# Optimization experiments

Hardware: AMD Instinct MI355X
Metric: run time of the kernel (lower is better)

Reference implementation:

```python
import jax, jax.numpy as jnp
import numpy as np
from jax import lax

V, D, H, K, B, T = 32000, 300, 300, 9, 64, 512


def _lstm_dir(x, w_ih, w_hh, b_ih, b_hh, h0, c0):
    # x: [B, T, D]; torch gate order: i, f, g, o
    def step(carry, xt):
        h, c = carry
        gates = xt @ w_ih.T + h @ w_hh.T + b_ih + b_hh  # [B, 4H]
        i, f, g, o = jnp.split(gates, 4, axis=-1)
        i, f, o = jax.nn.sigmoid(i), jax.nn.sigmoid(f), jax.nn.sigmoid(o)
        g = jnp.tanh(g)
        c = f * c + i * g
        h = o * jnp.tanh(c)
        return (h, c), h

    xs = jnp.transpose(x, (1, 0, 2))  # [T, B, D]
    _, hs = lax.scan(step, (h0, c0), xs)
    return jnp.transpose(hs, (1, 0, 2))  # [B, T, H]


def _emissions(tokens, emb, w_ih_f, w_hh_f, b_ih_f, b_hh_f,
               w_ih_b, w_hh_b, b_ih_b, b_hh_b, h0, c0, w_out, b_out):
    x = emb[tokens]  # [B, T, D]
    hf = _lstm_dir(x, w_ih_f, w_hh_f, b_ih_f, b_hh_f, h0[0], c0[0])
    hb = _lstm_dir(jnp.flip(x, axis=1), w_ih_b, w_hh_b, b_ih_b, b_hh_b, h0[1], c0[1])
    hb = jnp.flip(hb, axis=1)
    out = jnp.concatenate([hf, hb], axis=-1)  # [B, T, 2H]
    return out @ w_out.T + b_out  # [B, T, K]


def _crf_nll(emissions, tags, mask, start_t, end_t, trans):
    # torchcrf: -sum_b log p(tags | emissions)
    e = jnp.transpose(emissions, (1, 0, 2))  # [T, B, K]
    tg = tags.T                               # [T, B]
    m = mask.T.astype(emissions.dtype)        # [T, B]
    bidx = jnp.arange(tags.shape[0])
    # numerator: gold path score
    num = start_t[tg[0]] + e[0][bidx, tg[0]]
    def nstep(carry, inp):
        et, tt, tp, mt = inp
        return carry + (trans[tp, tt] + et[bidx, tt]) * mt, None
    num, _ = lax.scan(nstep, num, (e[1:], tg[1:], tg[:-1], m[1:]))
    last_idx = mask.sum(axis=1).astype(jnp.int32) - 1
    last_tags = tags[bidx, last_idx]
    num = num + end_t[last_tags]
    # denominator: forward algorithm
    alpha = start_t + e[0]  # [B, K]
    def dstep(alpha, inp):
        et, mt = inp
        nxt = jax.scipy.special.logsumexp(alpha[:, :, None] + trans[None], axis=1) + et
        return jnp.where(mt[:, None] > 0, nxt, alpha), None
    alpha, _ = lax.scan(dstep, alpha, (e[1:], m[1:]))
    den = jax.scipy.special.logsumexp(alpha + end_t, axis=1)
    return -jnp.sum(num - den)


def _viterbi(emissions, mask, start_t, end_t, trans):
    e = jnp.transpose(emissions, (1, 0, 2))  # [T, B, K]
    m = mask.T                               # [T, B]
    score = start_t + e[0]                   # [B, K]
    def fstep(score, inp):
        et, mt = inp
        br = score[:, :, None] + trans[None]  # [B, K_prev, K_next]
        best = br.max(axis=1)
        idx = br.argmax(axis=1).astype(jnp.int32)  # [B, K]
        new = best + et
        return jnp.where(mt[:, None], new, score), idx
    score, history = lax.scan(fstep, score, (e[1:], m[1:]))  # history: [T-1, B, K]
    score = score + end_t
    last = jnp.argmax(score, axis=-1).astype(jnp.int32)  # [B]
    def bstep(tag, inp):
        idx_t, mt = inp
        prev = jnp.take_along_axis(idx_t, tag[:, None], axis=1)[:, 0]
        tag = jnp.where(mt, prev, tag)
        return tag, tag
    _, tags_rev = lax.scan(bstep, last, (history, m[1:]), reverse=True)  # [T-1, B]
    path = jnp.concatenate([tags_rev, last[None]], axis=0)  # [T, B]
    return path.T  # [B, T]


def setup_inputs() -> dict:
    key = jax.random.key(0)
    ks = jax.random.split(key, 20)
    s = 0.1
    emb = jax.random.normal(ks[0], (V, D), jnp.float32) * s
    emb = emb.at[0].set(0.0)  # padding_idx row
    inp = {
        "tokens": jax.random.randint(ks[1], (B, T), 0, V, jnp.int32),
        "tags": jax.random.randint(ks[2], (B, T), 0, K, jnp.int32),
        "mask": jnp.ones((B, T), jnp.bool_),
        "emb": emb,
        "w_ih_f": jax.random.normal(ks[3], (4 * H, D), jnp.float32) * s,
        "w_hh_f": jax.random.normal(ks[4], (4 * H, H), jnp.float32) * s,
        "b_ih_f": jax.random.normal(ks[5], (4 * H,), jnp.float32) * s,
        "b_hh_f": jax.random.normal(ks[6], (4 * H,), jnp.float32) * s,
        "w_ih_b": jax.random.normal(ks[7], (4 * H, D), jnp.float32) * s,
        "w_hh_b": jax.random.normal(ks[8], (4 * H, H), jnp.float32) * s,
        "b_ih_b": jax.random.normal(ks[9], (4 * H,), jnp.float32) * s,
        "b_hh_b": jax.random.normal(ks[10], (4 * H,), jnp.float32) * s,
        "h0": jax.random.normal(ks[11], (2, B, H), jnp.float32),
        "c0": jax.random.normal(ks[12], (2, B, H), jnp.float32),
        "w_out": jax.random.normal(ks[13], (K, 2 * H), jnp.float32) * s,
        "b_out": jax.random.normal(ks[14], (K,), jnp.float32) * s,
        "start_t": jax.random.normal(ks[15], (K,), jnp.float32) * s,
        "end_t": jax.random.normal(ks[16], (K,), jnp.float32) * s,
        "trans": jax.random.normal(ks[17], (K, K), jnp.float32) * s,
    }
    return inp


def reference(tokens, tags, mask, emb, w_ih_f, w_hh_f, b_ih_f, b_hh_f,
              w_ih_b, w_hh_b, b_ih_b, b_hh_b, h0, c0, w_out, b_out,
              start_t, end_t, trans):
    feats = _emissions(tokens, emb, w_ih_f, w_hh_f, b_ih_f, b_hh_f,
                       w_ih_b, w_hh_b, b_ih_b, b_hh_b, h0, c0, w_out, b_out)
    paths = _viterbi(feats, mask, start_t, end_t, trans)
    loss = _crf_nll(feats, tags, mask, start_t, end_t, trans)
    return paths, loss
```

## Files before the change

### kernel.cpp

```cpp
#include <hip/hip_runtime.h>
#include <math.h>

#define NV 32000
#define ND 300
#define NH 300
#define NK 9
#define NB 64
#define NT 512

typedef short bf16x8 __attribute__((ext_vector_type(8)));
typedef float f32x4  __attribute__((ext_vector_type(4)));

__device__ inline short bf16r(float x) {
    return (short)((__float_as_uint(x) + 0x8000u) >> 16);
}

__device__ inline float tanh_fast(float x) {
    float e2 = __expf(2.f * x);
    return 1.f - 2.f / (e2 + 1.f);
}

#define WB_OFF   0ull
#define WB_F     768000ull
#define E_OFF    (WB_OFF + WB_F)
#define E_SZ     ((unsigned long long)NT*NB*NK)
#define CBUF_OFF (E_OFF + E_SZ)
#define CBUF_SZ  (2ull*NB*NH)
#define HSLOT_OFF (CBUF_OFF + CBUF_SZ)
#define HSLOT_SZ  (2ull*2*NB*NH)
#define XP_OFF   (HSLOT_OFF + HSLOT_SZ)
#define XPC_SZ   (2ull*64*1200*64)
#define EB_OFF   (XP_OFF + XPC_SZ)
#define EB_SZ    (32000ull*320/2)
#define WS_NEED_EB ((EB_OFF + EB_SZ)*4ull)

__global__ __launch_bounds__(256) void k_wcvt(
    const float* __restrict__ wihf, const float* __restrict__ wihb,
    const float* __restrict__ whhf, const float* __restrict__ whhb,
    short* __restrict__ dst)
{
    int i = blockIdx.x*256 + threadIdx.x;
    if (i >= 1536000) return;
    int d  = i / 384000;
    int r2 = i % 384000;
    int j  = r2 / 320, k = r2 % 320;
    const float* src = (d == 0) ? wihf : (d == 1) ? wihb : (d == 2) ? whhf : whhb;
    float v = (k < 300) ? src[(size_t)j*300 + k] : 0.f;
    dst[i] = bf16r(v);
}

__global__ __launch_bounds__(256) void k_ecvt(
    const float* __restrict__ emb, short* __restrict__ dst)
{
    int i = blockIdx.x*256 + threadIdx.x;
    if (i >= 32000*320) return;
    int row = i / 320, col = i % 320;
    float v = (col < 300) ? emb[(size_t)row*300 + col] : 0.f;
    dst[i] = bf16r(v);
}

__global__ __launch_bounds__(256) void k_xproj(
    const int* __restrict__ tokens, const float* __restrict__ emb,
    const short* __restrict__ eb16, int use_eb,
    const short* __restrict__ wb16,
    const float* __restrict__ bif, const float* __restrict__ bhf,
    const float* __restrict__ bib, const float* __restrict__ bhb,
    float* __restrict__ xpc, int chunk)
{
    const int tid = threadIdx.x;
    const int w  = tid >> 6, L = tid & 63;
    const int lm = L & 15, lq = L >> 4;
    const int dir = blockIdx.z;
    const int m0 = blockIdx.x*128 + w*32;
    const int n0 = blockIdx.y*80;
    const int tbase = dir ? (448 - chunk*64) : (chunk*64);

    int tok[2];
#pragma unroll
    for (int mi = 0; mi < 2; ++mi) {
        int m = m0 + mi*16 + lm;
        int b = m >> 6, lt = m & 63;
        tok[mi] = tokens[b*512 + tbase + lt];
    }
    const short* brow[5];
#pragma unroll
    for (int ni = 0; ni < 5; ++ni) {
        int j = n0 + ni*16 + lm;
        brow[ni] = wb16 + ((size_t)dir*1200 + j)*320;
    }

    f32x4 acc[2][5];
#pragma unroll
    for (int mi = 0; mi < 2; ++mi)
#pragma unroll
        for (int ni = 0; ni < 5; ++ni)
#pragma unroll
            for (int r = 0; r < 4; ++r) acc[mi][ni][r] = 0.f;

    if (use_eb) {
        const short* arow[2];
#pragma unroll
        for (int mi = 0; mi < 2; ++mi) arow[mi] = eb16 + (size_t)tok[mi]*320;
        for (int k0 = 0; k0 < 320; k0 += 32) {
            const int kk = k0 + lq*8;
            bf16x8 af[2], bf[5];
#pragma unroll
            for (int mi = 0; mi < 2; ++mi)
                af[mi] = *(const bf16x8*)(arow[mi] + kk);
#pragma unroll
            for (int ni = 0; ni < 5; ++ni)
                bf[ni] = *(const bf16x8*)(brow[ni] + kk);
#pragma unroll
            for (int mi = 0; mi < 2; ++mi)
#pragma unroll
                for (int ni = 0; ni < 5; ++ni)
                    acc[mi][ni] = __builtin_amdgcn_mfma_f32_16x16x32_bf16(
                                      af[mi], bf[ni], acc[mi][ni], 0, 0, 0);
        }
    } else {
        const float* arow[2];
#pragma unroll
        for (int mi = 0; mi < 2; ++mi) arow[mi] = emb + (size_t)tok[mi]*300;
        const float4 z4 = make_float4(0.f,0.f,0.f,0.f);
        for (int k0 = 0; k0 < 320; k0 += 32) {
            const int kk = k0 + lq*8;
            bf16x8 af[2], bf[5];
#pragma unroll
            for (int mi = 0; mi < 2; ++mi) {
                float4 f1 = (kk   < 300) ? *(const float4*)(arow[mi] + kk)     : z4;
                float4 f2 = (kk+4 < 300) ? *(const float4*)(arow[mi] + kk + 4) : z4;
                af[mi][0]=bf16r(f1.x); af[mi][1]=bf16r(f1.y); af[mi][2]=bf16r(f1.z); af[mi][3]=bf16r(f1.w);
                af[mi][4]=bf16r(f2.x); af[mi][5]=bf16r(f2.y); af[mi][6]=bf16r(f2.z); af[mi][7]=bf16r(f2.w);
            }
#pragma unroll
            for (int ni = 0; ni < 5; ++ni)
                bf[ni] = *(const bf16x8*)(brow[ni] + kk);
#pragma unroll
            for (int mi = 0; mi < 2; ++mi)
#pragma unroll
                for (int ni = 0; ni < 5; ++ni)
                    acc[mi][ni] = __builtin_amdgcn_mfma_f32_16x16x32_bf16(
                                      af[mi], bf[ni], acc[mi][ni], 0, 0, 0);
        }
    }

#pragma unroll
    for (int ni = 0; ni < 5; ++ni) {
        int j = n0 + ni*16 + lm;
        int g = j/300, rr = j%300;
        int slc = rr/20, ul = rr%20;
        float bias = dir ? (bib[j]+bhb[j]) : (bif[j]+bhf[j]);
#pragma unroll
        for (int mi = 0; mi < 2; ++mi) {
#pragma unroll
            for (int r = 0; r < 4; ++r) {
                int m = m0 + mi*16 + lq*4 + r;
                int b = m >> 6, lt = m & 63;
                int sp = dir ? (63 - lt) : lt;
                size_t idx = ((((size_t)dir*64 + sp)*8 + (b>>3))*15 + slc)*640
                           + (size_t)(b&7)*80 + g*20 + ul;
                xpc[idx] = acc[mi][ni][r] + bias;
            }
        }
    }
}

__global__ __launch_bounds__(256) void k_rnn(
    const float* __restrict__ xpc,
    const short* __restrict__ whh16,
    const float* __restrict__ h0,
    unsigned* hslot, float* __restrict__ cbuf,
    float* __restrict__ ev, const float* __restrict__ wout,
    int s_begin, int s_count)
{
    __shared__ __align__(16) short h_sh16[16*328];
    __shared__ __align__(16) float xp_sh[640];
    __shared__ __align__(16) float gates_sh[80*9];
    __shared__ __align__(16) float wo_sh[180];
    __shared__ __align__(16) float hloc[160];

    const int tid = threadIdx.x;
    const int wv  = tid >> 6, L = tid & 63;
    const int lm  = L & 15, lq = L >> 4;
    const int dir = blockIdx.x / 120;
    const int rem = blockIdx.x % 120;
    const int sl  = rem / 8;
    const int gb  = rem % 8;
    const int u0  = sl * 20;

    const int tb = (wv == 0) ? 0 : (wv + 1);
    const int tn = (wv == 0) ? 2 : 1;

    bf16x8 A[2][10];
#pragma unroll 2
    for (int mt = 0; mt < 2; ++mt) {
        if (mt < tn) {
            int r = (tb + mt)*16 + lm;
            int grow = (r/20)*300 + u0 + (r%20);
            const short* wr = whh16 + ((size_t)dir*1200 + grow)*320;
#pragma unroll
            for (int ks = 0; ks < 10; ++ks)
                A[mt][ks] = *(const bf16x8*)(wr + ks*32 + lq*8);
        }
    }
    if (tid < 180) wo_sh[tid] = wout[(tid/20)*600 + dir*300 + u0 + (tid%20)];

    for (int i = tid; i < 16*328; i += 256) h_sh16[i] = 0;

    const bool isPW = (tid < 160);
    const int bl_p = tid/20, lu_p = tid%20;
    float c_reg = 0.f;
    if (isPW) c_reg = cbuf[((size_t)dir*NB + gb*8 + bl_p)*NH + u0 + lu_p];

    __syncthreads();

    for (int s = s_begin; s < s_begin + s_count; ++s) {
        const int t = dir ? (511 - s) : s;
        const int sp = s - s_begin;

        unsigned vb[10];
        unsigned* hsrc = hslot + (((size_t)(s & 1)*2 + dir)*NB + gb*8)*NH;
        if (s > 0 && tid < 240) {
#pragma unroll
            for (int j = 0; j < 10; ++j) {
                int i = tid + 256*j;
                if (i < 2400)
                    vb[j] = __hip_atomic_load(hsrc + i, __ATOMIC_RELAXED,
                                              __HIP_MEMORY_SCOPE_AGENT);
            }
        }

        {
            const float* xsrc = xpc + ((((size_t)dir*64 + sp)*8 + gb)*15 + sl)*640;
            if (tid < 160) *(float4*)(&xp_sh[tid*4]) = *(const float4*)(xsrc + tid*4);
        }

        if (s == 0) {
            const float* h0p = h0 + ((size_t)dir*NB + gb*8)*NH;
            for (int i = tid; i < 2400; i += 256)
                h_sh16[(i/300)*328 + (i%300)] = bf16r(h0p[i]);
        } else if (tid < 240) {
            const unsigned tg = (unsigned)s & 0xFFFFu;
            bool ok = false;
            while (!ok) {
                ok = true;
#pragma unroll
                for (int j = 0; j < 10; ++j) {
                    int i = tid + 256*j;
                    if (i < 2400 && (vb[j] >> 16) != tg) {
                        ok = false;
                        vb[j] = __hip_atomic_load(hsrc + i, __ATOMIC_RELAXED,
                                                  __HIP_MEMORY_SCOPE_AGENT);
                    }
                }
            }
#pragma unroll
            for (int j = 0; j < 10; ++j) {
                int i = tid + 256*j;
                if (i < 2400)
                    h_sh16[(i/300)*328 + (i%300)] = (short)(vb[j] & 0xFFFFu);
            }
        }
        __syncthreads();

        {
            bf16x8 Bf[10];
#pragma unroll
            for (int ks = 0; ks < 10; ++ks)
                Bf[ks] = *(const bf16x8*)(h_sh16 + lm*328 + ks*32 + lq*8);
            f32x4 acc[2];
#pragma unroll 2
            for (int mt = 0; mt < 2; ++mt) {
                if (mt < tn) {
#pragma unroll
                    for (int r = 0; r < 4; ++r) acc[mt][r] = 0.f;
#pragma unroll
                    for (int ks = 0; ks < 10; ++ks)
                        acc[mt] = __builtin_amdgcn_mfma_f32_16x16x32_bf16(
                                      A[mt][ks], Bf[ks], acc[mt], 0, 0, 0);
                    if (lm < 8) {
#pragma unroll
                        for (int r = 0; r < 4; ++r)
                            gates_sh[((tb+mt)*16 + lq*4 + r)*9 + lm] = acc[mt][r];
                    }
                }
            }
        }
        __syncthreads();

        if (isPW) {
            float G[4];
#pragma unroll
            for (int g = 0; g < 4; ++g)
                G[g] = xp_sh[bl_p*80 + g*20 + lu_p] + gates_sh[(g*20 + lu_p)*9 + bl_p];
            float ig = 1.f/(1.f+__expf(-G[0]));
            float fg = 1.f/(1.f+__expf(-G[1]));
            float gg = tanh_fast(G[2]);
            float og = 1.f/(1.f+__expf(-G[3]));
            c_reg = fg*c_reg + ig*gg;
            float h = og*tanh_fast(c_reg);
            unsigned hb = (__float_as_uint(h) + 0x8000u) >> 16;
            unsigned pk = (((unsigned)(s+1) & 0xFFFFu) << 16) | hb;
            __hip_atomic_store(
                &hslot[(((size_t)((s+1)&1)*2 + dir)*NB + gb*8 + bl_p)*NH + u0 + lu_p],
                pk, __ATOMIC_RELAXED, __HIP_MEMORY_SCOPE_AGENT);
            hloc[bl_p*20 + lu_p] = h;
        }
        __syncthreads();

        if (tid < 72) {
            int b = tid/9, k = tid%9;
            float a = 0.f;
#pragma unroll
            for (int u = 0; u < 20; ++u) a += hloc[b*20+u]*wo_sh[k*20+u];
            atomicAdd(&ev[((size_t)t*NB + gb*8 + b)*NK + k], a);
        }
    }

    if (isPW) cbuf[((size_t)dir*NB + gb*8 + bl_p)*NH + u0 + lu_p] = c_reg;
}

#define BT_C 14
#define BT_L 37

__global__ __launch_bounds__(128) void k_crf(
    const float* __restrict__ ev, const int* __restrict__ tags,
    const float* __restrict__ start_t, const float* __restrict__ end_t,
    const float* __restrict__ trans, const float* __restrict__ bout,
    float* __restrict__ out)
{
    __shared__ __align__(16) float ex_a[12];
    __shared__ __align__(16) float ex_v[12];
    __shared__ int hist_sh[511*NK];
    __shared__ int fmap[BT_C*NK];
    __shared__ int entry_sh[BT_C];
    __shared__ int last_sh;

    const int b = blockIdx.x, tid = threadIdx.x;
    const int wv = tid >> 6, ln = tid & 63;

    if (wv == 0) {
        float part = 0.f;
        for (int t = ln; t < NT; t += 64) {
            int tc = tags[b*NT + t];
            float e = ev[((size_t)t*NB + b)*NK + tc] + bout[tc];
            float pre = (t == 0) ? start_t[tc] : trans[tags[b*NT + t - 1]*9 + tc];
            part += pre + e;
        }
        if (ln == 63) part += end_t[tags[b*NT + NT - 1]];
#pragma unroll
        for (int off = 32; off > 0; off >>= 1)
            part += __shfl_down(part, off, 64);
        const float num = part;

        if (ln < 9) {
            const int kc = ln;
            float Tc[9];
#pragma unroll
            for (int kp = 0; kp < 9; ++kp) Tc[kp] = __expf(trans[kp*9 + kc]);
            const float bo = bout[kc];
            ex_a[kc] = start_t[kc] + ev[(size_t)b*NK + kc] + bo;
            float etn = ev[((size_t)1*NB + b)*NK + kc] + bo;

            for (int t = 1; t < NT; ++t) {
                float et = etn;
                if (t + 1 < NT) etn = ev[((size_t)(t+1)*NB + b)*NK + kc] + bo;

                float4 s0 = *(const float4*)(&ex_a[0]);
                float4 s1 = *(const float4*)(&ex_a[4]);
                float  a8 = ex_a[8];
                float a0=s0.x,a1=s0.y,a2=s0.z,a3=s0.w,a4=s1.x,a5=s1.y,a6=s1.z,a7=s1.w;

                float M = fmaxf(fmaxf(fmaxf(a0,a1),fmaxf(a2,a3)),
                                fmaxf(fmaxf(a4,a5),fmaxf(a6,a7)));
                M = fmaxf(M, a8);
                float s =        __expf(a0-M)*Tc[0];
                s = fmaf(__expf(a1-M), Tc[1], s);
                s = fmaf(__expf(a2-M), Tc[2], s);
                s = fmaf(__expf(a3-M), Tc[3], s);
                s = fmaf(__expf(a4-M), Tc[4], s);
                s = fmaf(__expf(a5-M), Tc[5], s);
                s = fmaf(__expf(a6-M), Tc[6], s);
                s = fmaf(__expf(a7-M), Tc[7], s);
                s = fmaf(__expf(a8-M), Tc[8], s);
                ex_a[kc] = M + __logf(s) + et;
            }

            if (ln == 0) {
                float M = -1e30f;
#pragma unroll
                for (int k = 0; k < 9; ++k) M = fmaxf(M, ex_a[k] + end_t[k]);
                float ls = 0.f;
#pragma unroll
                for (int k = 0; k < 9; ++k) ls += __expf(ex_a[k] + end_t[k] - M);
                float den = M + __logf(ls);
                atomicAdd(out + NB*NT, den - num);
            }
        }
    } else {
        if (ln < 9) {
            const int kc = ln;
            float Tc[9];
#pragma unroll
            for (int kp = 0; kp < 9; ++kp) Tc[kp] = trans[kp*9 + kc];
            const float bo = bout[kc];
            ex_v[kc] = start_t[kc] + ev[(size_t)b*NK + kc] + bo;
            float etn = ev[((size_t)1*NB + b)*NK + kc] + bo;

            for (int t = 1; t < NT; ++t) {
                float et = etn;
                if (t + 1 < NT) etn = ev[((size_t)(t+1)*NB + b)*NK + kc] + bo;

                float4 s0 = *(const float4*)(&ex_v[0]);
                float4 s1 = *(const float4*)(&ex_v[4]);
                float  a8 = ex_v[8];
                float a0=s0.x,a1=s0.y,a2=s0.z,a3=s0.w,a4=s1.x,a5=s1.y,a6=s1.z,a7=s1.w;

                float bv = a0 + Tc[0]; int arg = 0;
                float v;
                v = a1+Tc[1]; if (v > bv) { bv = v; arg = 1; }
                v = a2+Tc[2]; if (v > bv) { bv = v; arg = 2; }
                v = a3+Tc[3]; if (v > bv) { bv = v; arg = 3; }
                v = a4+Tc[4]; if (v > bv) { bv = v; arg = 4; }
                v = a5+Tc[5]; if (v > bv) { bv = v; arg = 5; }
                v = a6+Tc[6]; if (v > bv) { bv = v; arg = 6; }
                v = a7+Tc[7]; if (v > bv) { bv = v; arg = 7; }
                v = a8+Tc[8]; if (v > bv) { bv = v; arg = 8; }
                hist_sh[(t-1)*NK + kc] = arg;
                ex_v[kc] = bv + et;
            }

            if (ln == 0) {
                float best = -1e30f; int last = 0;
#pragma unroll
                for (int k = 0; k < 9; ++k) {
                    float v = ex_v[k] + end_t[k];
                    if (v > best) { best = v; last = k; }
                }
                last_sh = last;
            }
        }
    }

    __syncthreads();

    if (tid < BT_C*NK) {
        int c = tid / NK, s = tid % NK;
        int lo = c*BT_L, hi = min(511, lo + BT_L);
        int pos = s;
        for (int i = hi - 1; i >= lo; --i) pos = hist_sh[i*NK + pos];
        fmap[c*NK + s] = pos;
    }
    __syncthreads();
    if (tid == 0) {
        int e = last_sh;
        entry_sh[BT_C-1] = e;
        for (int c = BT_C - 2; c >= 0; --c) {
            e = fmap[(c+1)*NK + e];
            entry_sh[c] = e;
        }
    }
    __syncthreads();
    int* pout = (int*)out;
    if (tid < BT_C) {
        int c = tid;
        int lo = c*BT_L, hi = min(511, lo + BT_L);
        int pos = entry_sh[c];
        for (int i = hi - 1; i >= lo; --i) {
            pos = hist_sh[i*NK + pos];
            pout[b*NT + i] = pos;
        }
    }
    if (tid == 0) pout[b*NT + NT - 1] = last_sh;
}

extern "C" void kernel_launch(void* const* d_in, const int* in_sizes, int n_in,
                              void* d_out, int out_size, void* d_ws, size_t ws_size,
                              hipStream_t stream)
{
    (void)in_sizes; (void)n_in;

    const int*   tokens = (const int*)  d_in[0];
    const int*   tags   = (const int*)  d_in[1];
    const float* emb    = (const float*)d_in[3];
    const float* wihf   = (const float*)d_in[4];
    const float* whhf   = (const float*)d_in[5];
    const float* bihf   = (const float*)d_in[6];
    const float* bhhf   = (const float*)d_in[7];
    const float* wihb   = (const float*)d_in[8];
    const float* whhb   = (const float*)d_in[9];
    const float* bib    = (const float*)d_in[10];
    const float* bhhb   = (const float*)d_in[11];
    const float* h0     = (const float*)d_in[12];
    const float* c0     = (const float*)d_in[13];
    const float* wout   = (const float*)d_in[14];
    const float* bout   = (const float*)d_in[15];
    const float* startt = (const float*)d_in[16];
    const float* endt   = (const float*)d_in[17];
    const float* trans  = (const float*)d_in[18];

    float* ws    = (float*)d_ws;
    short* wb16  = (short*)(ws + WB_OFF);
    short* whh16 = wb16 + 768000;
    float* evp   = ws + E_OFF;
    float* cbuf  = ws + CBUF_OFF;
    unsigned* hslot = (unsigned*)(ws + HSLOT_OFF);
    float* xp    = ws + XP_OFF;
    short* eb16  = (short*)(ws + EB_OFF);
    float* out   = (float*)d_out;

    const int use_eb = (ws_size >= WS_NEED_EB) ? 1 : 0;

    (void)hipMemsetAsync(d_out, 0, (size_t)out_size * sizeof(float), stream);
    (void)hipMemsetAsync(evp, 0, (size_t)E_SZ * sizeof(float), stream);
    (void)hipMemcpyAsync(cbuf, c0, 2ull*NB*NH*sizeof(float), hipMemcpyDeviceToDevice, stream);

    k_wcvt<<<6000, 256, 0, stream>>>(wihf, wihb, whhf, whhb, wb16);
    if (use_eb)
        k_ecvt<<<40000, 256, 0, stream>>>(emb, eb16);

    for (int c = 0; c < 8; ++c) {
        k_xproj<<<dim3(32, 15, 2), 256, 0, stream>>>(
            tokens, emb, eb16, use_eb, wb16, bihf, bhhf, bib, bhhb, xp, c);
        k_rnn<<<240, 256, 0, stream>>>(
            xp, whh16, h0, hslot, cbuf, evp, wout, c*64, 64);
    }
    k_crf<<<64, 128, 0, stream>>>(evp, tags, startt, endt, trans, bout, out);
}
```

Before: 1.876 ms.

## Parallelize CRF forward and Viterbi recursions over time chunks with transfer matrices

Splits the 511-step CRF forward (logsumexp) and Viterbi (max-plus) recursions into 8 time chunks of 64 steps. Each chunk computes a 9x9 transfer matrix in parallel, one thread per start state. A single thread then composes the chunk matrices, and each chunk's Viterbi is replayed from the composed entry scores to fill the backpointer history in parallel. This targets the serial latency of the CRF kernel, but adds roughly 9x redundant arithmetic per chunk and an extra replay pass. It also doubles the block size to 256 threads.

```diff
diff --git a/kernel.cpp b/kernel.cpp
--- a/kernel.cpp
+++ b/kernel.cpp
@@ -322,98 +322,221 @@
 
 #define BT_C 14
 #define BT_L 37
-
-__global__ __launch_bounds__(128) void k_crf(
+#define CC 8
+#define CL 64
+
+__global__ __launch_bounds__(256) void k_crf(
     const float* __restrict__ ev, const int* __restrict__ tags,
     const float* __restrict__ start_t, const float* __restrict__ end_t,
     const float* __restrict__ trans, const float* __restrict__ bout,
     float* __restrict__ out)
 {
-    __shared__ __align__(16) float ex_a[12];
-    __shared__ __align__(16) float ex_v[12];
     __shared__ int hist_sh[511*NK];
+    __shared__ float Mlse[CC*81];
+    __shared__ float Mvit[CC*81];
+    __shared__ float entry_v[CC*9];
+    __shared__ __align__(16) float ex3[CC*12];
+    __shared__ float num_sh[256];
     __shared__ int fmap[BT_C*NK];
     __shared__ int entry_sh[BT_C];
     __shared__ int last_sh;
 
     const int b = blockIdx.x, tid = threadIdx.x;
-    const int wv = tid >> 6, ln = tid & 63;
-
-    if (wv == 0) {
+    const int wv = tid >> 6;
+
+    {
         float part = 0.f;
-        for (int t = ln; t < NT; t += 64) {
+        for (int t = tid; t < NT; t += 256) {
             int tc = tags[b*NT + t];
             float e = ev[((size_t)t*NB + b)*NK + tc] + bout[tc];
             float pre = (t == 0) ? start_t[tc] : trans[tags[b*NT + t - 1]*9 + tc];
             part += pre + e;
-        }
-        if (ln == 63) part += end_t[tags[b*NT + NT - 1]];
-#pragma unroll
-        for (int off = 32; off > 0; off >>= 1)
-            part += __shfl_down(part, off, 64);
-        const float num = part;
-
-        if (ln < 9) {
-            const int kc = ln;
+            if (t == NT - 1) part += end_t[tc];
+        }
+        num_sh[tid] = part;
+    }
+
+    {
+        int c = -1, j0 = 0, sr = 0;
+        if (wv == 0)      { if (tid < 63)        { c = tid/9;        j0 = tid%9;        sr = 0; } }
+        else if (wv == 1) { if (tid-64 < 63)     { c = (tid-64)/9;   j0 = (tid-64)%9;   sr = 1; } }
+        else if (wv == 2) { if (tid-128 < 9)     { c = 7;            j0 = tid-128;      sr = 0; } }
+        else              { if (tid-192 < 9)     { c = 7;            j0 = tid-192;      sr = 1; } }
+
+        if (c >= 0 && sr == 0) {
+            float Te[9][9];
+#pragma unroll
+            for (int i = 0; i < 9; ++i)
+#pragma unroll
+                for (int j = 0; j < 9; ++j) Te[i][j] = __expf(trans[i*9 + j]);
+            float bo[9];
+#pragma unroll
+            for (int j = 0; j < 9; ++j) bo[j] = bout[j];
+            float a[9];
+#pragma unroll
+            for (int j = 0; j < 9; ++j) a[j] = (j == j0) ? 0.f : -1e30f;
+            const int t0 = 1 + c*CL;
+            float etn[9];
+#pragma unroll
+            for (int j = 0; j < 9; ++j)
+                etn[j] = ev[((size_t)t0*NB + b)*NK + j] + bo[j];
+            for (int k = 0; k < CL; ++k) {
+                int t = t0 + k;
+                if (t >= NT) break;
+                float et[9];
+#pragma unroll
+                for (int j = 0; j < 9; ++j) et[j] = etn[j];
+                if (t + 1 < NT) {
+#pragma unroll
+                    for (int j = 0; j < 9; ++j)
+                        etn[j] = ev[((size_t)(t+1)*NB + b)*NK + j] + bo[j];
+                }
+                float M = a[0];
+#pragma unroll
+                for (int i = 1; i < 9; ++i) M = fmaxf(M, a[i]);
+                float p[9];
+#pragma unroll
+                for (int i = 0; i < 9; ++i) p[i] = __expf(a[i] - M);
+#pragma unroll
+                for (int j = 0; j < 9; ++j) {
+                    float s = p[0]*Te[0][j];
+#pragma unroll
+                    for (int i = 1; i < 9; ++i) s = fmaf(p[i], Te[i][j], s);
+                    a[j] = M + __logf(s) + et[j];
+                }
+            }
+#pragma unroll
+            for (int j = 0; j < 9; ++j) Mlse[c*81 + j0*9 + j] = a[j];
+        } else if (c >= 0) {
+            float Tv[9][9];
+#pragma unroll
+            for (int i = 0; i < 9; ++i)
+#pragma unroll
+                for (int j = 0; j < 9; ++j) Tv[i][j] = trans[i*9 + j];
+            float bo[9];
+#pragma unroll
+            for (int j = 0; j < 9; ++j) bo[j] = bout[j];
+            float a[9];
+#pragma unroll
+            for (int j = 0; j < 9; ++j) a[j] = (j == j0) ? 0.f : -1e30f;
+            const int t0 = 1 + c*CL;
+            float etn[9];
+#pragma unroll
+            for (int j = 0; j < 9; ++j)
+                etn[j] = ev[((size_t)t0*NB + b)*NK + j] + bo[j];
+            for (int k = 0; k < CL; ++k) {
+                int t = t0 + k;
+                if (t >= NT) break;
+                float et[9];
+#pragma unroll
+                for (int j = 0; j < 9; ++j) et[j] = etn[j];
+                if (t + 1 < NT) {
+#pragma unroll
+                    for (int j = 0; j < 9; ++j)
+                        etn[j] = ev[((size_t)(t+1)*NB + b)*NK + j] + bo[j];
+                }
+                float an[9];
+#pragma unroll
+                for (int j = 0; j < 9; ++j) {
+                    float bv = a[0] + Tv[0][j];
+#pragma unroll
+                    for (int i = 1; i < 9; ++i) bv = fmaxf(bv, a[i] + Tv[i][j]);
+                    an[j] = bv + et[j];
+                }
+#pragma unroll
+                for (int j = 0; j < 9; ++j) a[j] = an[j];
+            }
+#pragma unroll
+            for (int j = 0; j < 9; ++j) Mvit[c*81 + j0*9 + j] = a[j];
+        }
+    }
+    __syncthreads();
+
+    if (tid == 0) {
+        float num = 0.f;
+        for (int i = 0; i < 256; ++i) num += num_sh[i];
+        float al[9];
+#pragma unroll
+        for (int j = 0; j < 9; ++j)
+            al[j] = start_t[j] + ev[(size_t)b*NK + j] + bout[j];
+        for (int c = 0; c < CC; ++c) {
+            float an[9];
+#pragma unroll
+            for (int j = 0; j < 9; ++j) {
+                float m = al[0] + Mlse[c*81 + 0*9 + j];
+#pragma unroll
+                for (int i = 1; i < 9; ++i)
+                    m = fmaxf(m, al[i] + Mlse[c*81 + i*9 + j]);
+                float s = 0.f;
+#pragma unroll
+                for (int i = 0; i < 9; ++i)
+                    s += __expf(al[i] + Mlse[c*81 + i*9 + j] - m);
+                an[j] = m + __logf(s);
+            }
+#pragma unroll
+            for (int j = 0; j < 9; ++j) al[j] = an[j];
+        }
+        float M = al[0] + end_t[0];
+#pragma unroll
+        for (int j = 1; j < 9; ++j) M = fmaxf(M, al[j] + end_t[j]);
+        float ls = 0.f;
+#pragma unroll
+        for (int j = 0; j < 9; ++j) ls += __expf(al[j] + end_t[j] - M);
+        float den = M + __logf(ls);
+        atomicAdd(out + NB*NT, den - num);
+    }
+    if (tid == 64) {
+        float av[9];
+#pragma unroll
+        for (int j = 0; j < 9; ++j)
+            av[j] = start_t[j] + ev[(size_t)b*NK + j] + bout[j];
+        for (int c = 0; c < CC; ++c) {
+#pragma unroll
+            for (int j = 0; j < 9; ++j) entry_v[c*9 + j] = av[j];
+            float an[9];
+#pragma unroll
+            for (int j = 0; j < 9; ++j) {
+                float bv = av[0] + Mvit[c*81 + 0*9 + j];
+#pragma unroll
+                for (int i = 1; i < 9; ++i)
+                    bv = fmaxf(bv, av[i] + Mvit[c*81 + i*9 + j]);
+                an[j] = bv;
+            }
+#pragma unroll
+            for (int j = 0; j < 9; ++j) av[j] = an[j];
+        }
+        float best = av[0] + end_t[0]; int last = 0;
+#pragma unroll
+        for (int j = 1; j < 9; ++j) {
+            float v = av[j] + end_t[j];
+            if (v > best) { best = v; last = j; }
+        }
+        last_sh = last;
+    }
+    __syncthreads();
+
+    {
+        int c = -1, j3 = 0;
+        if (wv == 0)      { if (tid < 63)    { c = tid/9;  j3 = tid%9;  } }
+        else if (wv == 1) { if (tid-64 < 9)  { c = 7;      j3 = tid-64; } }
+        if (c >= 0) {
             float Tc[9];
 #pragma unroll
-            for (int kp = 0; kp < 9; ++kp) Tc[kp] = __expf(trans[kp*9 + kc]);
-            const float bo = bout[kc];
-            ex_a[kc] = start_t[kc] + ev[(size_t)b*NK + kc] + bo;
-            float etn = ev[((size_t)1*NB + b)*NK + kc] + bo;
-
-            for (int t = 1; t < NT; ++t) {
+            for (int i = 0; i < 9; ++i) Tc[i] = trans[i*9 + j3];
+            const float bo3 = bout[j3];
+            ex3[c*12 + j3] = entry_v[c*9 + j3];
+            const int t0 = 1 + c*CL;
+            float etn = ev[((size_t)t0*NB + b)*NK + j3] + bo3;
+            for (int k = 0; k < CL; ++k) {
+                int t = t0 + k;
+                if (t >= NT) break;
                 float et = etn;
-                if (t + 1 < NT) etn = ev[((size_t)(t+1)*NB + b)*NK + kc] + bo;
-
-                float4 s0 = *(const float4*)(&ex_a[0]);
-                float4 s1 = *(const float4*)(&ex_a[4]);
-                float  a8 = ex_a[8];
-                float a0=s0.x,a1=s0.y,a2=s0.z,a3=s0.w,a4=s1.x,a5=s1.y,a6=s1.z,a7=s1.w;
-
-                float M = fmaxf(fmaxf(fmaxf(a0,a1),fmaxf(a2,a3)),
-                                fmaxf(fmaxf(a4,a5),fmaxf(a6,a7)));
-                M = fmaxf(M, a8);
-                float s =        __expf(a0-M)*Tc[0];
-                s = fmaf(__expf(a1-M), Tc[1], s);
-                s = fmaf(__expf(a2-M), Tc[2], s);
-                s = fmaf(__expf(a3-M), Tc[3], s);
-                s = fmaf(__expf(a4-M), Tc[4], s);
-                s = fmaf(__expf(a5-M), Tc[5], s);
-                s = fmaf(__expf(a6-M), Tc[6], s);
-                s = fmaf(__expf(a7-M), Tc[7], s);
-                s = fmaf(__expf(a8-M), Tc[8], s);
-                ex_a[kc] = M + __logf(s) + et;
-            }
-
-            if (ln == 0) {
-                float M = -1e30f;
-#pragma unroll
-                for (int k = 0; k < 9; ++k) M = fmaxf(M, ex_a[k] + end_t[k]);
-                float ls = 0.f;
-#pragma unroll
-                for (int k = 0; k < 9; ++k) ls += __expf(ex_a[k] + end_t[k] - M);
-                float den = M + __logf(ls);
-                atomicAdd(out + NB*NT, den - num);
-            }
-        }
-    } else {
-        if (ln < 9) {
-            const int kc = ln;
-            float Tc[9];
-#pragma unroll
-            for (int kp = 0; kp < 9; ++kp) Tc[kp] = trans[kp*9 + kc];
-            const float bo = bout[kc];
-            ex_v[kc] = start_t[kc] + ev[(size_t)b*NK + kc] + bo;
-            float etn = ev[((size_t)1*NB + b)*NK + kc] + bo;
-
-            for (int t = 1; t < NT; ++t) {
-                float et = etn;
-                if (t + 1 < NT) etn = ev[((size_t)(t+1)*NB + b)*NK + kc] + bo;
-
-                float4 s0 = *(const float4*)(&ex_v[0]);
-                float4 s1 = *(const float4*)(&ex_v[4]);
-                float  a8 = ex_v[8];
+                if (t + 1 < NT)
+                    etn = ev[((size_t)(t+1)*NB + b)*NK + j3] + bo3;
+
+                float4 s0 = *(const float4*)(&ex3[c*12]);
+                float4 s1 = *(const float4*)(&ex3[c*12 + 4]);
+                float  a8 = ex3[c*12 + 8];
                 float a0=s0.x,a1=s0.y,a2=s0.z,a3=s0.w,a4=s1.x,a5=s1.y,a6=s1.z,a7=s1.w;
 
                 float bv = a0 + Tc[0]; int arg = 0;
@@ -426,22 +549,11 @@
                 v = a6+Tc[6]; if (v > bv) { bv = v; arg = 6; }
                 v = a7+Tc[7]; if (v > bv) { bv = v; arg = 7; }
                 v = a8+Tc[8]; if (v > bv) { bv = v; arg = 8; }
-                hist_sh[(t-1)*NK + kc] = arg;
-                ex_v[kc] = bv + et;
-            }
-
-            if (ln == 0) {
-                float best = -1e30f; int last = 0;
-#pragma unroll
-                for (int k = 0; k < 9; ++k) {
-                    float v = ex_v[k] + end_t[k];
-                    if (v > best) { best = v; last = k; }
-                }
-                last_sh = last;
-            }
-        }
-    }
-
+                hist_sh[(t-1)*NK + j3] = arg;
+                ex3[c*12 + j3] = bv + et;
+            }
+        }
+    }
     __syncthreads();
 
     if (tid < BT_C*NK) {
@@ -525,5 +637,5 @@
         k_rnn<<<240, 256, 0, stream>>>(
             xp, whh16, h0, hslot, cbuf, evp, wout, c*64, 64);
     }
-    k_crf<<<64, 128, 0, stream>>>(evp, tags, startt, endt, trans, bout, out);
-}
+    k_crf<<<64, 256, 0, stream>>>(evp, tags, startt, endt, trans, bout, out);
+}
```

After: 1.789 ms. 4.6% less time.
